# Kernel tuning notes

Measured on AMD Instinct MI355X. Metric: run time of the kernel, lower is better.

Reference implementation:

```python
import jax, jax.numpy as jnp
import numpy as np

N_HEAD = 16
D_HEAD = 64
D_MODEL = 1024
SCALE = 1.0 / D_HEAD ** 0.5


def setup_inputs() -> dict:
    key = jax.random.key(0)
    k1, k2 = jax.random.split(key)
    h = jax.random.normal(k1, (2048, 2, D_MODEL), dtype=jnp.float32)
    # torch Linear weight layout: [out_features, in_features]
    w_qkv = jax.random.normal(k2, (3 * N_HEAD * D_HEAD, D_MODEL), dtype=jnp.float32) * (D_MODEL ** -0.5)
    return {"h": h, "w_qkv": w_qkv}


def reference(h, w_qkv):
    qlen, bsz, _ = h.shape
    heads = h @ w_qkv.T  # [qlen, bsz, 3*n_head*d_head]
    head_q, head_k, head_v = jnp.split(heads, 3, axis=-1)
    head_q = head_q.reshape(qlen, bsz, N_HEAD, D_HEAD)
    head_k = head_k.reshape(qlen, bsz, N_HEAD, D_HEAD)
    head_v = head_v.reshape(qlen, bsz, N_HEAD, D_HEAD)
    attn_score = jnp.einsum('ibnd,jbnd->ijbn', head_q, head_k) * SCALE
    attn_prob = jax.nn.softmax(attn_score, axis=1)  # softmax over key dim j
    # dropout is identity at p=0.0 / eval mode
    attn_vec = jnp.einsum('ijbn,jbnd->ibnd', attn_prob, head_v)
    attn_vec = attn_vec.reshape(qlen, bsz, N_HEAD * D_HEAD)
    return attn_vec, attn_prob
```

## Files before the change

### kernel.cpp

```cpp
#include <hip/hip_runtime.h>

typedef _Float16 f16;
typedef f16 f16x8 __attribute__((ext_vector_type(8)));
typedef f16 f16x4 __attribute__((ext_vector_type(4)));
typedef float f32x4 __attribute__((ext_vector_type(4)));

#define QLEN 2048
#define BSZ 2
#define NH 16
#define DH 64
#define DM 1024
#define NBN (BSZ*NH)
#define SCALE 0.125f
#define QPRESCALE (0.125f * 1.44269504f)

static __device__ __forceinline__ f32x4 mfma16(f16x8 a, f16x8 b, f32x4 c) {
  return __builtin_amdgcn_mfma_f32_16x16x32_f16(a, b, c, 0, 0, 0);
}

static __device__ __forceinline__ void gload_lds16(const void* g, void* l) {
  __builtin_amdgcn_global_load_lds((const __attribute__((address_space(1))) unsigned int*)g,
                                   (__attribute__((address_space(3))) unsigned int*)l,
                                   16, 0, 0);
}

static __device__ __forceinline__ void barrier_lds() {
  __builtin_amdgcn_sched_barrier(0);
  asm volatile("s_waitcnt lgkmcnt(0)");
  __builtin_amdgcn_s_barrier();
  __builtin_amdgcn_sched_barrier(0);
}

__global__ __launch_bounds__(256) void cvt_f32_f16(const float* __restrict__ s,
                                                   f16* __restrict__ d, int n4) {
  int idx = blockIdx.x * 256 + threadIdx.x;
  if (idx >= n4) return;
  f32x4 v = ((const f32x4*)s)[idx];
  f16x4 o;
#pragma unroll
  for (int q = 0; q < 4; ++q) o[q] = (f16)v[q];
  ((f16x4*)d)[idx] = o;
}

__global__ __launch_bounds__(256) void qkv_gemm(const f16* __restrict__ A, const f16* __restrict__ W,
                                                f16* __restrict__ Qs, f16* __restrict__ Ks,
                                                f16* __restrict__ Vt) {
  __shared__ f16 S[16384];
  f16* As = S;
  f16* Bs = S + 4096;
  const int bid = blockIdx.x;
  const int r0 = (bid & 31) << 7;
  const int c0 = (bid >> 5) << 7;
  const int t = threadIdx.x;
  const int lane = t & 63, w = t >> 6;
  const int wr = (w >> 1) << 6, wc = (w & 1) << 6;
  const int l15 = lane & 15, lhi = lane >> 4;

  f32x4 acc[4][4] = {};

  const f16* ga = A + (size_t)(r0 + (t >> 2)) * DM + ((t & 3) << 3);
  const f16* gb = W + (size_t)(c0 + (t >> 2)) * DM + ((t & 3) << 3);
  char* la = (char*)As + w * 1024;
  char* lb = (char*)Bs + w * 1024;

  for (int k0 = 0; k0 < DM; k0 += 32) {
    __syncthreads();
    gload_lds16(ga + k0, la);
    gload_lds16(ga + k0 + (size_t)64 * DM, la + 4096);
    gload_lds16(gb + k0, lb);
    gload_lds16(gb + k0 + (size_t)64 * DM, lb + 4096);
    __syncthreads();
    f16x8 af[4], bf[4];
#pragma unroll
    for (int m = 0; m < 4; ++m)
      af[m] = *(const f16x8*)&As[(wr + m * 16 + l15) * 32 + lhi * 8];
#pragma unroll
    for (int n = 0; n < 4; ++n)
      bf[n] = *(const f16x8*)&Bs[(wc + n * 16 + l15) * 32 + lhi * 8];
#pragma unroll
    for (int m = 0; m < 4; ++m)
#pragma unroll
      for (int n = 0; n < 4; ++n)
        acc[m][n] = mfma16(af[m], bf[n], acc[m][n]);
  }

  const int part = c0 >> 10;
  const int nh_base = (c0 >> 6) & 15;
  const int i0g = r0 >> 1;
  const float qs = (part == 0) ? QPRESCALE : 1.0f;

  __syncthreads();

#pragma unroll
  for (int m = 0; m < 4; ++m)
#pragma unroll
    for (int n = 0; n < 4; ++n)
#pragma unroll
      for (int q = 0; q < 4; ++q) {
        const int r_l = wr + m * 16 + lhi * 4 + q;
        const int c_l = wc + n * 16 + l15;
        const int i = r_l >> 1;
        const int d = c_l & 63;
        const int bn2 = ((r_l & 1) << 1) + (c_l >> 6);
        const f16 v = (f16)(acc[m][n][q] * qs);
        if (part < 2)
          S[(bn2 * 64 + i) * 64 + ((((d >> 3) ^ (i & 7)) << 3) | (d & 7))] = v;
        else
          S[(bn2 * 64 + d) * 64 + ((((i >> 3) ^ (d & 7)) << 3) | (i & 7))] = v;
      }
  __syncthreads();

  {
    const int bn2 = t >> 6;
    const int row7 = (t >> 3) & 7;
    const int o8 = t & 7;
    const int bn = ((bn2 >> 1) << 4) + nh_base + (bn2 & 1);
#pragma unroll
    for (int c = 0; c < 8; ++c) {
      const int row = row7 + c * 8;
      f16x8 v = *(const f16x8*)&S[(bn2 * 64 + row) * 64 + ((o8 ^ (row & 7)) << 3)];
      f16* dst;
      if (part == 0)      dst = Qs + ((size_t)bn * QLEN + i0g + row) * DH + o8 * 8;
      else if (part == 1) dst = Ks + ((size_t)bn * QLEN + i0g + row) * DH + o8 * 8;
      else                dst = Vt + ((size_t)bn * DH + row) * QLEN + i0g + o8 * 8;
      *(f16x8*)dst = v;
    }
  }
}

__global__ __launch_bounds__(256) void flash_attn(const f16* __restrict__ Qs, const f16* __restrict__ Ks,
                                                  const f16* __restrict__ Vt, float* __restrict__ av,
                                                  float* __restrict__ srl) {
  __shared__ f16 plds[4][16 * 40];
  const int bid = blockIdx.x;
  const int bn = bid & 31, ib = bid >> 5;
  const int t = threadIdx.x, lane = t & 63, w = t >> 6;
  const int l15 = lane & 15, lhi = lane >> 4;
  const int i0 = (ib << 7) + (w << 5);
  const f16* Qb = Qs + ((size_t)bn << 17);
  const f16* Kb = Ks + ((size_t)bn << 17);
  const f16* Vb = Vt + ((size_t)bn << 17);
  f16* pw = plds[w];

  f16x8 qf[2][2];
#pragma unroll
  for (int rg = 0; rg < 2; ++rg)
#pragma unroll
    for (int kc = 0; kc < 2; ++kc)
      qf[rg][kc] = *(const f16x8*)&Qb[(size_t)(i0 + rg * 16 + l15) * DH + kc * 32 + lhi * 8];

  f32x4 o[2][4] = {};
  float psum[2] = {};

  for (int j0 = 0; j0 < QLEN; j0 += 32) {
    f16x8 kf[2][2], vf[4];
#pragma unroll
    for (int jc = 0; jc < 2; ++jc)
#pragma unroll
      for (int kc = 0; kc < 2; ++kc)
        kf[jc][kc] = *(const f16x8*)&Kb[(size_t)(j0 + jc * 16 + l15) * DH + kc * 32 + lhi * 8];
#pragma unroll
    for (int dc = 0; dc < 4; ++dc)
      vf[dc] = *(const f16x8*)&Vb[(size_t)(dc * 16 + l15) * QLEN + j0 + lhi * 8];

#pragma unroll
    for (int rg = 0; rg < 2; ++rg) {
      f32x4 zt[2];
#pragma unroll
      for (int jc = 0; jc < 2; ++jc) {
        f32x4 z = {0.f, 0.f, 0.f, 0.f};
        z = mfma16(kf[jc][0], qf[rg][0], z);
        z = mfma16(kf[jc][1], qf[rg][1], z);
        zt[jc] = z;
      }
      f16x4 pk[2];
      float ls = 0.f;
#pragma unroll
      for (int jc = 0; jc < 2; ++jc)
#pragma unroll
        for (int q = 0; q < 4; ++q) {
          float p = exp2f(zt[jc][q]);
          ls += p;
          pk[jc][q] = (f16)p;
        }
      psum[rg] += ls;
#pragma unroll
      for (int jc = 0; jc < 2; ++jc)
        *(f16x4*)&pw[l15 * 40 + jc * 16 + lhi * 4] = pk[jc];
      f16x8 pa = *(const f16x8*)&pw[l15 * 40 + lhi * 8];
#pragma unroll
      for (int dc = 0; dc < 4; ++dc)
        o[rg][dc] = mfma16(pa, vf[dc], o[rg][dc]);
    }
  }

  float lrun[2], rn[2][4];
#pragma unroll
  for (int rg = 0; rg < 2; ++rg) {
    float r = psum[rg];
    r += __shfl_xor(r, 16);
    r += __shfl_xor(r, 32);
    lrun[rg] = r;
#pragma unroll
    for (int q = 0; q < 4; ++q)
      rn[rg][q] = __shfl(lrun[rg], lhi * 4 + q);
  }

  const int b = bn >> 4, nh = bn & 15;
#pragma unroll
  for (int rg = 0; rg < 2; ++rg)
#pragma unroll
    for (int dc = 0; dc < 4; ++dc)
#pragma unroll
      for (int q = 0; q < 4; ++q) {
        int i = i0 + rg * 16 + lhi * 4 + q;
        av[((size_t)i * BSZ + b) * (NH * DH) + nh * DH + dc * 16 + l15] =
            o[rg][dc][q] / rn[rg][q];
      }
  if (lhi == 0) {
#pragma unroll
    for (int rg = 0; rg < 2; ++rg)
      srl[bn * QLEN + i0 + rg * 16 + l15] = 1.0f / lrun[rg];
  }
}

#define LOADK(buf, chn)                                                        \
  do {                                                                         \
    _Pragma("unroll") for (int bl_ = 0; bl_ < 4; ++bl_) {                      \
      const f16* Kb_ = Ks + (((size_t)(w4 + bl_)) << 17) +                     \
                       (size_t)(j0 + (chn) * 16 + l15) * DH + lhi * 8;         \
      buf[bl_][0] = *(const f16x8*)(Kb_);                                      \
      buf[bl_][1] = *(const f16x8*)(Kb_ + 32);                                 \
    }                                                                          \
  } while (0)

#define SUBCHUNK(cur, nxt, ch, sub)                                            \
  do {                                                                         \
    f16 stv[4][4];                                                             \
    _Pragma("unroll") for (int bl_ = 0; bl_ < 4; ++bl_) {                      \
      f32x4 z = {0.f, 0.f, 0.f, 0.f};                                          \
      z = mfma16(qf[bl_][0], cur[bl_][0], z);                                  \
      z = mfma16(qf[bl_][1], cur[bl_][1], z);                                  \
      _Pragma("unroll") for (int q_ = 0; q_ < 4; ++q_)                         \
        stv[bl_][q_] = (f16)(exp2f(z[q_]) * rl[bl_][q_]);                      \
    }                                                                          \
    __builtin_amdgcn_sched_barrier(0);                                         \
    { const int nch_ = ((ch) + 1 < 16) ? (ch) + 1 : 15; LOADK(nxt, nch_); }    \
    __builtin_amdgcn_sched_barrier(0);                                         \
    _Pragma("unroll") for (int q_ = 0; q_ < 4; ++q_) {                         \
      const int i_l = lhi * 4 + q_;                                            \
      const int jl = (sub) * 16 + l15;                                         \
      f16x4 v = {stv[0][q_], stv[1][q_], stv[2][q_], stv[3][q_]};              \
      *(f16x4*)&tile[(i_l * 64 + jl) * 32 + ((w ^ (l15 & 7)) << 2)] = v;       \
    }                                                                          \
  } while (0)

__global__ __launch_bounds__(512, 1) void write_probs(const f16* __restrict__ Qs, const f16* __restrict__ Ks,
                                                      const float* __restrict__ srl,
                                                      float* __restrict__ pout) {
  __shared__ f16 tile[16 * 64 * 32];
  const int bid = blockIdx.x;
  const int it = bid >> 3, jt = bid & 7;
  const int i0 = it << 4, j0 = jt << 8;
  const int t = threadIdx.x, lane = t & 63, w = t >> 6;
  const int l15 = lane & 15, lhi = lane >> 4;
  const int w4 = w * 4;

  f16x8 qf[4][2];
  float rl[4][4];
#pragma unroll
  for (int bl = 0; bl < 4; ++bl) {
    const int bn = w4 + bl;
    const f16* Qb = Qs + ((size_t)bn << 17);
#pragma unroll
    for (int kc = 0; kc < 2; ++kc)
      qf[bl][kc] = *(const f16x8*)&Qb[(size_t)(i0 + l15) * DH + kc * 32 + lhi * 8];
#pragma unroll
    for (int q = 0; q < 4; ++q)
      rl[bl][q] = srl[bn * QLEN + i0 + lhi * 4 + q];
  }

  const int j_s = t >> 3;
  const int o = t & 7;
  const int swz = o ^ (j_s & 7);

  f16x8 kfA[4][2], kfB[4][2];
  LOADK(kfA, 0);

  for (int ph = 0; ph < 4; ++ph) {
    const int c0 = ph * 4;
    SUBCHUNK(kfA, kfB, c0 + 0, 0);
    SUBCHUNK(kfB, kfA, c0 + 1, 1);
    SUBCHUNK(kfA, kfB, c0 + 2, 2);
    SUBCHUNK(kfB, kfA, c0 + 3, 3);
    barrier_lds();
#pragma unroll
    for (int r = 0; r < 16; ++r) {
      f16x4 v = *(const f16x4*)&tile[(r * 64 + j_s) * 32 + (swz << 2)];
      f32x4 ov = {(float)v[0], (float)v[1], (float)v[2], (float)v[3]};
      float* op = pout + ((size_t)(i0 + r) * QLEN + j0 + ph * 64 + j_s) * NBN + o * 4;
      __builtin_nontemporal_store(ov, (f32x4*)op);
    }
    barrier_lds();
  }
}

extern "C" void kernel_launch(void* const* d_in, const int* in_sizes, int n_in,
                              void* d_out, int out_size, void* d_ws, size_t ws_size,
                              hipStream_t stream) {
  const float* h  = (const float*)d_in[0];
  const float* wq = (const float*)d_in[1];
  float* av   = (float*)d_out;
  float* pout = av + (size_t)QLEN * BSZ * NH * DH;

  char* ws = (char*)d_ws;
  f16* hh  = (f16*)ws;
  f16* wh  = (f16*)(ws + (8u << 20));
  f16* Qsc = (f16*)(ws + (16u << 20));
  f16* Ksc = (f16*)(ws + (24u << 20));
  f16* Vtc = (f16*)(ws + (32u << 20));
  float* srlv = (float*)(ws + (40u << 20));

  const int nh4 = QLEN * BSZ * DM / 4;
  const int nw4 = 3 * NH * DH * DM / 4;
  cvt_f32_f16<<<nh4 / 256, 256, 0, stream>>>(h, hh, nh4);
  cvt_f32_f16<<<nw4 / 256, 256, 0, stream>>>(wq, wh, nw4);
  qkv_gemm<<<32 * 24, 256, 0, stream>>>(hh, wh, Qsc, Ksc, Vtc);
  flash_attn<<<NBN * 16, 256, 0, stream>>>(Qsc, Ksc, Vtc, av, srlv);
  write_probs<<<128 * 8, 512, 0, stream>>>(Qsc, Ksc, srlv, pout);
}
```

Before: 324.4 us.

## Halve write_probs block size, give each wave eight heads, drop K prefetch

The write_probs kernel now runs with 256 threads (4 waves) per block instead of 512, and each wave computes eight batch-head slices instead of four. Launch bounds allow two blocks per CU. The double-buffered K register prefetch with sched barriers is replaced by a plain load-then-compute per subchunk. The goal is to let two blocks share a CU so one block's LDS transpose and stores overlap the other's compute, at the cost of more registers per wave and losing the explicit K prefetch.

```diff
diff --git a/kernel.cpp b/kernel.cpp
--- a/kernel.cpp
+++ b/kernel.cpp
@@ -90,7 +90,6 @@
   const float qs = (part == 0) ? QPRESCALE : 1.0f;
 
   __syncthreads();
-
 #pragma unroll
   for (int m = 0; m < 4; ++m)
 #pragma unroll
@@ -224,38 +223,7 @@
   }
 }
 
-#define LOADK(buf, chn)                                                        \
-  do {                                                                         \
-    _Pragma("unroll") for (int bl_ = 0; bl_ < 4; ++bl_) {                      \
-      const f16* Kb_ = Ks + (((size_t)(w4 + bl_)) << 17) +                     \
-                       (size_t)(j0 + (chn) * 16 + l15) * DH + lhi * 8;         \
-      buf[bl_][0] = *(const f16x8*)(Kb_);                                      \
-      buf[bl_][1] = *(const f16x8*)(Kb_ + 32);                                 \
-    }                                                                          \
-  } while (0)
-
-#define SUBCHUNK(cur, nxt, ch, sub)                                            \
-  do {                                                                         \
-    f16 stv[4][4];                                                             \
-    _Pragma("unroll") for (int bl_ = 0; bl_ < 4; ++bl_) {                      \
-      f32x4 z = {0.f, 0.f, 0.f, 0.f};                                          \
-      z = mfma16(qf[bl_][0], cur[bl_][0], z);                                  \
-      z = mfma16(qf[bl_][1], cur[bl_][1], z);                                  \
-      _Pragma("unroll") for (int q_ = 0; q_ < 4; ++q_)                         \
-        stv[bl_][q_] = (f16)(exp2f(z[q_]) * rl[bl_][q_]);                      \
-    }                                                                          \
-    __builtin_amdgcn_sched_barrier(0);                                         \
-    { const int nch_ = ((ch) + 1 < 16) ? (ch) + 1 : 15; LOADK(nxt, nch_); }    \
-    __builtin_amdgcn_sched_barrier(0);                                         \
-    _Pragma("unroll") for (int q_ = 0; q_ < 4; ++q_) {                         \
-      const int i_l = lhi * 4 + q_;                                            \
-      const int jl = (sub) * 16 + l15;                                         \
-      f16x4 v = {stv[0][q_], stv[1][q_], stv[2][q_], stv[3][q_]};              \
-      *(f16x4*)&tile[(i_l * 64 + jl) * 32 + ((w ^ (l15 & 7)) << 2)] = v;       \
-    }                                                                          \
-  } while (0)
-
-__global__ __launch_bounds__(512, 1) void write_probs(const f16* __restrict__ Qs, const f16* __restrict__ Ks,
+__global__ __launch_bounds__(256, 2) void write_probs(const f16* __restrict__ Qs, const f16* __restrict__ Ks,
                                                       const float* __restrict__ srl,
                                                       float* __restrict__ pout) {
   __shared__ f16 tile[16 * 64 * 32];
@@ -264,13 +232,13 @@
   const int i0 = it << 4, j0 = jt << 8;
   const int t = threadIdx.x, lane = t & 63, w = t >> 6;
   const int l15 = lane & 15, lhi = lane >> 4;
-  const int w4 = w * 4;
-
-  f16x8 qf[4][2];
-  float rl[4][4];
-#pragma unroll
-  for (int bl = 0; bl < 4; ++bl) {
-    const int bn = w4 + bl;
+  const int w8 = w * 8;
+
+  f16x8 qf[8][2];
+  float rl[8][4];
+#pragma unroll
+  for (int bl = 0; bl < 8; ++bl) {
+    const int bn = w8 + bl;
     const f16* Qb = Qs + ((size_t)bn << 17);
 #pragma unroll
     for (int kc = 0; kc < 2; ++kc)
@@ -280,26 +248,58 @@
       rl[bl][q] = srl[bn * QLEN + i0 + lhi * 4 + q];
   }
 
-  const int j_s = t >> 3;
+  const int j_lo = t >> 3;
   const int o = t & 7;
-  const int swz = o ^ (j_s & 7);
-
-  f16x8 kfA[4][2], kfB[4][2];
-  LOADK(kfA, 0);
 
   for (int ph = 0; ph < 4; ++ph) {
-    const int c0 = ph * 4;
-    SUBCHUNK(kfA, kfB, c0 + 0, 0);
-    SUBCHUNK(kfB, kfA, c0 + 1, 1);
-    SUBCHUNK(kfA, kfB, c0 + 2, 2);
-    SUBCHUNK(kfB, kfA, c0 + 3, 3);
+    const int jbase = j0 + ph * 64;
+
+#pragma unroll
+    for (int sub = 0; sub < 4; ++sub) {
+      f16x8 kf[8][2];
+#pragma unroll
+      for (int bl = 0; bl < 8; ++bl) {
+        const f16* Kb = Ks + (((size_t)(w8 + bl)) << 17) +
+                        (size_t)(jbase + sub * 16 + l15) * DH + lhi * 8;
+        kf[bl][0] = *(const f16x8*)(Kb);
+        kf[bl][1] = *(const f16x8*)(Kb + 32);
+      }
+      f16 stv[8][4];
+#pragma unroll
+      for (int bl = 0; bl < 8; ++bl) {
+        f32x4 z = {0.f, 0.f, 0.f, 0.f};
+        z = mfma16(qf[bl][0], kf[bl][0], z);
+        z = mfma16(qf[bl][1], kf[bl][1], z);
+#pragma unroll
+        for (int q = 0; q < 4; ++q)
+          stv[bl][q] = (f16)(exp2f(z[q]) * rl[bl][q]);
+      }
+#pragma unroll
+      for (int h = 0; h < 2; ++h) {
+        const int g = w * 2 + h;
+#pragma unroll
+        for (int q = 0; q < 4; ++q) {
+          const int i_l = lhi * 4 + q;
+          const int jl = sub * 16 + l15;
+          f16x4 v = {stv[4 * h + 0][q], stv[4 * h + 1][q],
+                     stv[4 * h + 2][q], stv[4 * h + 3][q]};
+          *(f16x4*)&tile[(i_l * 64 + jl) * 32 + ((g ^ (jl & 7)) << 2)] = v;
+        }
+      }
+    }
     barrier_lds();
+
 #pragma unroll
     for (int r = 0; r < 16; ++r) {
-      f16x4 v = *(const f16x4*)&tile[(r * 64 + j_s) * 32 + (swz << 2)];
-      f32x4 ov = {(float)v[0], (float)v[1], (float)v[2], (float)v[3]};
-      float* op = pout + ((size_t)(i0 + r) * QLEN + j0 + ph * 64 + j_s) * NBN + o * 4;
-      __builtin_nontemporal_store(ov, (f32x4*)op);
+#pragma unroll
+      for (int h = 0; h < 2; ++h) {
+        const int j_s = h * 32 + j_lo;
+        const int swz = o ^ (j_s & 7);
+        f16x4 v = *(const f16x4*)&tile[(r * 64 + j_s) * 32 + (swz << 2)];
+        f32x4 ov = {(float)v[0], (float)v[1], (float)v[2], (float)v[3]};
+        float* op = pout + ((size_t)(i0 + r) * QLEN + jbase + j_s) * NBN + o * 4;
+        __builtin_nontemporal_store(ov, (f32x4*)op);
+      }
     }
     barrier_lds();
   }
@@ -327,5 +327,5 @@
   cvt_f32_f16<<<nw4 / 256, 256, 0, stream>>>(wq, wh, nw4);
   qkv_gemm<<<32 * 24, 256, 0, stream>>>(hh, wh, Qsc, Ksc, Vtc);
   flash_attn<<<NBN * 16, 256, 0, stream>>>(Qsc, Ksc, Vtc, av, srlv);
-  write_probs<<<128 * 8, 512, 0, stream>>>(Qsc, Ksc, srlv, pout);
-}
+  write_probs<<<128 * 8, 256, 0, stream>>>(Qsc, Ksc, srlv, pout);
+}
```

Result: no change. 327.6 us (+1.0%).
